# Optimization experiments

Measured on AMD Instinct MI355X. Metric: run time of the kernel, lower is better.

Reference implementation:

```python
import jax, jax.numpy as jnp
import numpy as np
import math

MU = 5; ETA = 1.0; ITERS = 3
SIGMA_C = 1.0; SIGMA_S = 1.6 * SIGMA_C
SIGMA_M = 3.0; RHO = 0.99; TAU = 0.7
MAX_T = int(math.floor(3 * SIGMA_C))  # 3
MAX_S = int(math.floor(3 * SIGMA_M))  # 9
DELTA = 1.0
B, C, X, Y = 4, 1, 512, 512


def _gpdf(v, sig):
    return math.exp(-v * v / (2.0 * sig * sig)) / (math.sqrt(2.0 * math.pi) * sig)


def _sobel(img):
    k = jnp.array([[-1., -2., -1.], [0., 0., 0.], [1., 2., 1.]], dtype=img.dtype)
    kern = jnp.stack([k, k.T])[:, None]  # [2,1,3,3] OIHW
    return jax.lax.conv_general_dilated(img, kern, (1, 1), [(1, 1), (1, 1)],
                                        dimension_numbers=('NCHW', 'OIHW', 'NCHW'))


def _gather_flat(arr, idx):
    # arr [b,c,x,y], idx int [b,x,y] flattened spatial index (px*Y+py)
    b, c, x, y = arr.shape
    flat = arr.reshape(b, c, x * y)
    idxb = jnp.broadcast_to(idx.reshape(b, 1, x * y), (b, c, x * y))
    return jnp.take_along_axis(flat, idxb, axis=2).reshape(b, c, x, y)


def _safe_norm(v):
    m = jnp.linalg.norm(v, axis=1, keepdims=True)
    return v / jnp.where(m == 0, 1.0, m)


def _etf(images):
    b, c, x, y = images.shape
    sob = _sobel(images)                                   # [b,2,x,y]
    mag = jnp.linalg.norm(sob, axis=1, keepdims=True)      # [b,1,x,y]
    mag = mag / jnp.max(mag)
    mag_p = jnp.pad(mag, ((0, 0), (0, 0), (MU, MU), (MU, MU)))
    sobel_X = mag[:, None]                                 # [b,1,1,x,y]
    tang = _safe_norm(jnp.stack([-sob[:, 1], sob[:, 0]], axis=1))
    K = 2 * MU + 1
    for _ in range(ITERS):
        for ori in ('V', 'H'):
            tang_p = jnp.pad(tang, ((0, 0), (0, 0), (MU, MU), (MU, MU)))
            tang_X = tang[:, None]                         # [b,1,2,x,y]
            if ori == 'V':
                tang_Y = jnp.stack([tang_p[:, :, i:i + x, MU:MU + y] for i in range(K)], axis=1)
                sobel_Y = jnp.stack([mag_p[:, :, i:i + x, MU:MU + y] for i in range(K)], axis=1)
            else:
                tang_Y = jnp.stack([tang_p[:, :, MU:MU + x, i:i + y] for i in range(K)], axis=1)
                sobel_Y = jnp.stack([mag_p[:, :, MU:MU + x, i:i + y] for i in range(K)], axis=1)
            # weight: magnitude term * direction term / 2
            w = (jnp.tanh(ETA * (sobel_Y - sobel_X)) + 1.0) \
                * jnp.sum(tang_X * tang_Y, axis=2, keepdims=True) * 0.5
            tang = _safe_norm(jnp.sum(tang_Y * w, axis=1))
    return tang


def _dog(images, etf):
    b, c, x, y = images.shape
    xi, yi = jnp.meshgrid(jnp.arange(x, dtype=images.dtype),
                          jnp.arange(y, dtype=images.dtype), indexing='ij')
    idx0 = jnp.broadcast_to(jnp.stack([xi, yi])[None], (b, 2, x, y))
    per = jnp.stack([-etf[:, 1], etf[:, 0]], axis=1)       # perpendicular to flow
    dog = jnp.zeros_like(images)
    tw = 0.0
    for t in range(-MAX_T, MAX_T + 1):
        pts = idx0 + DELTA * per * t
        px = jnp.round(jnp.clip(pts[:, 0], 0, x - 1)).astype(jnp.int32)
        py = jnp.round(jnp.clip(pts[:, 1], 0, y - 1)).astype(jnp.int32)
        il = _gather_flat(images, px * y + py)
        gw = _gpdf(t, SIGMA_C) - RHO * _gpdf(t, SIGMA_S)
        tw += gw
        dog = dog + il * gw
    return dog / tw


def _fdog_float(images):
    b, c, x, y = images.shape
    etf = _etf(images)
    dog = _dog(images, etf)
    fdog = jnp.zeros_like(images)
    tw = 0.0
    xi, yi = jnp.meshgrid(jnp.arange(x, dtype=jnp.int32),
                          jnp.arange(y, dtype=jnp.int32), indexing='ij')
    for s_dir in (-1, 1):
        px = jnp.broadcast_to(xi[None], (b, x, y))
        py = jnp.broadcast_to(yi[None], (b, x, y))
        for s in range(0 if s_dir == 1 else 1, MAX_S + 1):
            if s != 0:
                p_etf = _gather_flat(etf, px * y + py)     # flow at current points
                fx = px.astype(images.dtype) + DELTA * p_etf[:, 0] * s_dir
                fy = py.astype(images.dtype) + DELTA * p_etf[:, 1] * s_dir
                px = jnp.round(jnp.clip(fx, 0, x - 1)).astype(jnp.int32)
                py = jnp.round(jnp.clip(fy, 0, y - 1)).astype(jnp.int32)
            f_s = _gather_flat(dog, px * y + py)
            gw = _gpdf(s, SIGMA_M)
            tw += gw
            fdog = fdog + f_s * gw
    return fdog / tw


def setup_inputs() -> dict:
    key = jax.random.key(0)
    images = jax.random.uniform(key, (B, C, X, Y), dtype=jnp.float32)
    return {"images": images}


def reference(images):
    fdog = _fdog_float(images)
    edges = ~((fdog < 0) & (1.0 + jnp.tanh(fdog) < TAU))
    return edges.astype(jnp.int32)
```

## Files before the change

kernel.cpp:

```cpp
#include <hip/hip_runtime.h>
#include <math.h>

#pragma clang fp contract(off)

#define BN 4
#define SX 512
#define SY 512
#define NPIX (BN * SX * SY)
#define MU 5
#define MB (1024 * 1024)
#define NBLOCKS 4096

struct DogW  { float g[7];  float tw; };
struct FdogW { float g[10]; float tw; };

__device__ __forceinline__ float fast_tanh_f32(float dF) {
    double d = (double)dF;
    double y = fabs(d);
    double t = expm1(2.0 * y);
    double r = t / (t + 2.0);
    if (y > 350.0) r = 1.0;
    return (float)copysign(r, d);
}

__device__ __forceinline__ float img_at(const float* __restrict__ img, int b, int x, int y) {
    if (x < 0 || x >= SX || y < 0 || y >= SY) return 0.0f;
    return img[(size_t)b * SX * SY + (size_t)x * SY + y];
}

__global__ void k_sobel(const float* __restrict__ img, float* __restrict__ mag,
                        float2* __restrict__ tang, float* __restrict__ partial) {
#pragma clang fp contract(off)
    int yi = blockIdx.x * blockDim.x + threadIdx.x;
    int xi = blockIdx.y;
    int b  = blockIdx.z;

    float v00 = img_at(img, b, xi - 1, yi - 1);
    float v01 = img_at(img, b, xi - 1, yi    );
    float v02 = img_at(img, b, xi - 1, yi + 1);
    float v10 = img_at(img, b, xi,     yi - 1);
    float v12 = img_at(img, b, xi,     yi + 1);
    float v20 = img_at(img, b, xi + 1, yi - 1);
    float v21 = img_at(img, b, xi + 1, yi    );
    float v22 = img_at(img, b, xi + 1, yi + 1);

    float s0 = (-1.0f * v00);
    s0 = s0 + (-2.0f * v01);
    s0 = s0 + (-1.0f * v02);
    s0 = s0 + ( 1.0f * v20);
    s0 = s0 + ( 2.0f * v21);
    s0 = s0 + ( 1.0f * v22);
    float s1 = (-1.0f * v00);
    s1 = s1 + ( 1.0f * v02);
    s1 = s1 + (-2.0f * v10);
    s1 = s1 + ( 2.0f * v12);
    s1 = s1 + (-1.0f * v20);
    s1 = s1 + ( 1.0f * v22);

    float m = sqrtf((s0 * s0) + (s1 * s1));
    size_t idx = (size_t)b * SX * SY + (size_t)xi * SY + yi;
    mag[idx] = m;

    float tx = -s1, ty = s0;
    float n = sqrtf((tx * tx) + (ty * ty));
    float d = (n == 0.0f) ? 1.0f : n;
    tang[idx] = make_float2(tx / d, ty / d);

    float wm = m;
    for (int off = 32; off > 0; off >>= 1) wm = fmaxf(wm, __shfl_down(wm, off, 64));
    __shared__ float red[4];
    int lane = threadIdx.x & 63;
    int wid  = threadIdx.x >> 6;
    if (lane == 0) red[wid] = wm;
    __syncthreads();
    if (threadIdx.x == 0) {
        float bm = fmaxf(fmaxf(red[0], red[1]), fmaxf(red[2], red[3]));
        int bid = blockIdx.x + gridDim.x * (blockIdx.y + gridDim.y * blockIdx.z);
        partial[bid] = bm;
    }
}

__global__ void k_reduce(const float* __restrict__ partial, unsigned int* __restrict__ maxbits) {
    float m = 0.0f;
    for (int i = threadIdx.x; i < NBLOCKS; i += 256) m = fmaxf(m, partial[i]);
    for (int off = 32; off > 0; off >>= 1) m = fmaxf(m, __shfl_down(m, off, 64));
    __shared__ float red[4];
    int lane = threadIdx.x & 63;
    int wid  = threadIdx.x >> 6;
    if (lane == 0) red[wid] = m;
    __syncthreads();
    if (threadIdx.x == 0) {
        float bm = fmaxf(fmaxf(red[0], red[1]), fmaxf(red[2], red[3]));
        *maxbits = __float_as_uint(bm);
    }
}

__global__ void k_norm(float* __restrict__ mag, const unsigned int* __restrict__ maxbits) {
    int i = blockIdx.x * blockDim.x + threadIdx.x;
    float mx = __uint_as_float(*maxbits);
    mag[i] = mag[i] / mx;
}

__global__ void k_tanh(const float* __restrict__ mag, const unsigned int* __restrict__ maxbits,
                       float* __restrict__ TV, float* __restrict__ TH) {
#pragma clang fp contract(off)
    int yi = blockIdx.x * blockDim.x + threadIdx.x;
    int xi = blockIdx.y;
    int b  = blockIdx.z;
    size_t base = (size_t)b * SX * SY;
    size_t idx  = base + (size_t)xi * SY + yi;
    float mx = __uint_as_float(*maxbits);
    float cm = mag[idx] / mx;
#pragma unroll
    for (int k = 1; k <= 5; ++k) {
        if (xi + k < SX) {
            float nm = mag[idx + (size_t)k * SY] / mx;
            TV[(size_t)(k - 1) * NPIX + idx] = fast_tanh_f32(nm - cm);
        }
    }
#pragma unroll
    for (int k = 1; k <= 5; ++k) {
        if (yi + k < SY) {
            float nm = mag[idx + k] / mx;
            TH[(size_t)(k - 1) * NPIX + idx] = fast_tanh_f32(nm - cm);
        }
    }
}

#define VTY 32
#define VTX 8
__global__ __launch_bounds__(256) void k_etf_v(const float2* __restrict__ tsrc,
                                               float2* __restrict__ tdst,
                                               const float* __restrict__ TV) {
#pragma clang fp contract(off)
    int ty = threadIdx.x & 31;
    int tx = threadIdx.x >> 5;
    int y0 = blockIdx.x * VTY;
    int x0 = blockIdx.y * VTX;
    int b  = blockIdx.z;
    size_t base = (size_t)b * SX * SY;

    __shared__ __align__(16) float2 sT[VTX + 2 * MU][VTY];
    __shared__ __align__(16) float  sTV[5][VTX + MU][VTY];

    int tid = threadIdx.x;
    for (int i = tid; i < (VTX + 2 * MU) * (VTY / 2) / 2; i += 256) {
        break;
    }
    for (int i = tid; i < (VTX + 2 * MU) * (VTY / 4) * 2; i += 256) {
        int r = i >> 4;
        int c = i & 15;
        int gx = x0 - MU + r;
        if (gx >= 0 && gx < SX)
            ((float4*)&sT[r][0])[c] = ((const float4*)(tsrc + base + (size_t)gx * SY + y0))[c];
    }
    for (int i = tid; i < 5 * (VTX + MU) * (VTY / 4); i += 256) {
        int j   = i / ((VTX + MU) * (VTY / 4));
        int rem = i - j * ((VTX + MU) * (VTY / 4));
        int r   = rem >> 3;
        int c   = rem & 7;
        int gx  = x0 - MU + r;
        if (gx >= 0 && gx < SX)
            ((float4*)&sTV[j][r][0])[c] =
                ((const float4*)(TV + (size_t)j * NPIX + base + (size_t)gx * SY + y0))[c];
    }
    __syncthreads();

    int xi = x0 + tx;
    int yi = y0 + ty;
    size_t idx = base + (size_t)xi * SY + yi;

    float2 ct = sT[tx + MU][ty];

    float sx = 0.0f, sy = 0.0f;
#pragma unroll
    for (int k = -MU; k <= MU; ++k) {
        int nx = xi + k;
        if (nx < 0 || nx >= SX) continue;
        float2 nt = sT[tx + MU + k][ty];
        float th;
        if (k > 0)      th =  sTV[k - 1][tx + MU][ty];
        else if (k < 0) th = -sTV[-k - 1][tx + MU + k][ty];
        else            th =  0.0f;
        float dot = (ct.x * nt.x) + (ct.y * nt.y);
        float w   = ((th + 1.0f) * dot) * 0.5f;
        sx = sx + (nt.x * w);
        sy = sy + (nt.y * w);
    }
    float n = sqrtf((sx * sx) + (sy * sy));
    float d = (n == 0.0f) ? 1.0f : n;
    tdst[idx] = make_float2(sx / d, sy / d);
}

__global__ __launch_bounds__(256) void k_etf_h(const float2* __restrict__ tsrc,
                                               float2* __restrict__ tdst,
                                               const float* __restrict__ TH) {
#pragma clang fp contract(off)
    int tid = threadIdx.x;
    int xi  = blockIdx.y;
    int b   = blockIdx.z;
    size_t rowbase = (size_t)b * SX * SY + (size_t)xi * SY;

    __shared__ __align__(16) float2 sT[SY];
    __shared__ __align__(16) float  sTH[5][SY];

    ((float4*)sT)[tid] = ((const float4*)(tsrc + rowbase))[tid];
    for (int i = tid; i < 5 * (SY / 4); i += 256) {
        int j = i >> 7;
        int c = i & 127;
        ((float4*)&sTH[0][0])[i] = ((const float4*)(TH + (size_t)j * NPIX + rowbase))[c];
    }
    __syncthreads();

#pragma unroll
    for (int half = 0; half < 2; ++half) {
        int yi = tid + half * 256;
        float2 ct = sT[yi];
        float sx = 0.0f, sy = 0.0f;
#pragma unroll
        for (int k = -MU; k <= MU; ++k) {
            int ny = yi + k;
            if (ny < 0 || ny >= SY) continue;
            float2 nt = sT[ny];
            float th;
            if (k > 0)      th =  sTH[k - 1][yi];
            else if (k < 0) th = -sTH[-k - 1][ny];
            else            th =  0.0f;
            float dot = (ct.x * nt.x) + (ct.y * nt.y);
            float w   = ((th + 1.0f) * dot) * 0.5f;
            sx = sx + (nt.x * w);
            sy = sy + (nt.y * w);
        }
        float n = sqrtf((sx * sx) + (sy * sy));
        float d = (n == 0.0f) ? 1.0f : n;
        tdst[rowbase + yi] = make_float2(sx / d, sy / d);
    }
}

__global__ void k_etf(const float2* __restrict__ tsrc, float2* __restrict__ tdst,
                      const float* __restrict__ mag, int vert) {
#pragma clang fp contract(off)
    int yi = blockIdx.x * blockDim.x + threadIdx.x;
    int xi = blockIdx.y;
    int b  = blockIdx.z;
    size_t base = (size_t)b * SX * SY;
    size_t idx  = base + (size_t)xi * SY + yi;

    float  cm = mag[idx];
    float2 ct = tsrc[idx];

    float sx = 0.0f, sy = 0.0f;
    for (int k = -MU; k <= MU; ++k) {
        int nx = xi + (vert ? k : 0);
        int ny = yi + (vert ? 0 : k);
        if (nx < 0 || nx >= SX || ny < 0 || ny >= SY) continue;
        size_t nidx = base + (size_t)nx * SY + ny;
        float  nm = mag[nidx];
        float2 nt = tsrc[nidx];
        float dot = (ct.x * nt.x) + (ct.y * nt.y);
        float th  = (float)tanh((double)(nm - cm));
        float w   = ((th + 1.0f) * dot) * 0.5f;
        sx = sx + (nt.x * w);
        sy = sy + (nt.y * w);
    }
    float n = sqrtf((sx * sx) + (sy * sy));
    float d = (n == 0.0f) ? 1.0f : n;
    tdst[idx] = make_float2(sx / d, sy / d);
}

__global__ void k_dog(const float* __restrict__ img, const float2* __restrict__ etf,
                      float* __restrict__ dog, DogW w) {
#pragma clang fp contract(off)
    int yi = blockIdx.x * blockDim.x + threadIdx.x;
    int xi = blockIdx.y;
    int b  = blockIdx.z;
    size_t base = (size_t)b * SX * SY;
    size_t idx  = base + (size_t)xi * SY + yi;

    float2 e = etf[idx];
    float perx = -e.y;
    float pery =  e.x;
    float xf = (float)xi, yf = (float)yi;

    float acc = 0.0f;
#pragma unroll
    for (int t = -3; t <= 3; ++t) {
        float tf  = (float)t;
        float ptx = xf + (perx * tf);
        float pty = yf + (pery * tf);
        int px = (int)rintf(fminf(fmaxf(ptx, 0.0f), (float)(SX - 1)));
        int py = (int)rintf(fminf(fmaxf(pty, 0.0f), (float)(SY - 1)));
        float il = img[base + (size_t)px * SY + py];
        acc = acc + (il * w.g[t + 3]);
    }
    dog[idx] = acc / w.tw;
}

__global__ void k_fdog(const float* __restrict__ dog, const float2* __restrict__ etf,
                       int* __restrict__ out, FdogW w) {
#pragma clang fp contract(off)
    int yi = blockIdx.x * blockDim.x + threadIdx.x;
    int xi = blockIdx.y;
    int b  = blockIdx.z;
    size_t base = (size_t)b * SX * SY;
    size_t idx  = base + (size_t)xi * SY + yi;

    float d1[9];
    float d2[10];
    float2 e0 = etf[idx];
    float2 e1 = e0, e2 = e0;
    int p1x = xi, p1y = yi;
    int p2x = xi, p2y = yi;
    d2[0] = dog[idx];

#pragma unroll
    for (int s = 1; s <= 9; ++s) {
        float fx1 = (float)p1x + (e1.x * -1.0f);
        float fy1 = (float)p1y + (e1.y * -1.0f);
        p1x = (int)rintf(fminf(fmaxf(fx1, 0.0f), (float)(SX - 1)));
        p1y = (int)rintf(fminf(fmaxf(fy1, 0.0f), (float)(SY - 1)));
        size_t i1 = base + (size_t)p1x * SY + p1y;
        float fx2 = (float)p2x + (e2.x * 1.0f);
        float fy2 = (float)p2y + (e2.y * 1.0f);
        p2x = (int)rintf(fminf(fmaxf(fx2, 0.0f), (float)(SX - 1)));
        p2y = (int)rintf(fminf(fmaxf(fy2, 0.0f), (float)(SY - 1)));
        size_t i2 = base + (size_t)p2x * SY + p2y;

        d1[s - 1] = dog[i1];
        d2[s]     = dog[i2];
        if (s < 9) {
            e1 = etf[i1];
            e2 = etf[i2];
        }
    }

    float acc = 0.0f;
#pragma unroll
    for (int s = 1; s <= 9; ++s) acc = acc + (d1[s - 1] * w.g[s]);
    acc = acc + (d2[0] * w.g[0]);
#pragma unroll
    for (int s = 1; s <= 9; ++s) acc = acc + (d2[s] * w.g[s]);

    float fv = acc / w.tw;
    float th = 1.0f + fast_tanh_f32(fv);
    out[idx] = ((fv < 0.0f) && (th < 0.7f)) ? 0 : 1;
}

static double gpdf(double v, double sig) {
    return exp(-(v * v) / (2.0 * sig * sig)) / (sqrt(2.0 * M_PI) * sig);
}

extern "C" void kernel_launch(void* const* d_in, const int* in_sizes, int n_in,
                              void* d_out, int out_size, void* d_ws, size_t ws_size,
                              hipStream_t stream) {
    const float* img = (const float*)d_in[0];
    int* out = (int*)d_out;
    char* ws = (char*)d_ws;

    const size_t need = (size_t)60 * MB + NBLOCKS * sizeof(float) + 4;
    bool fast = ws_size >= need;

    float*  mag = (float*)(ws);
    float2* tA  = (float2*)(ws + (size_t)4  * MB);
    float2* tB  = (float2*)(ws + (size_t)12 * MB);
    float*  dog = (float*)(ws + (size_t)12 * MB);
    float*  TV  = (float*)(ws + (size_t)20 * MB);
    float*  TH  = (float*)(ws + (size_t)40 * MB);
    size_t  tail = fast ? (size_t)60 * MB : (size_t)20 * MB;
    float*        partial = (float*)(ws + tail);
    unsigned int* maxbits = (unsigned int*)(ws + tail + NBLOCKS * sizeof(float));

    dim3 blk(256, 1, 1);
    dim3 grd(SY / 256, SX, BN);
    dim3 vgrd(SY / VTY, SX / VTX, BN);
    dim3 hgrd(1, SX, BN);

    k_sobel<<<grd, blk, 0, stream>>>(img, mag, tA, partial);
    k_reduce<<<1, 256, 0, stream>>>(partial, maxbits);

    float2* src = tA;
    float2* dst = tB;
    if (fast) {
        k_tanh<<<grd, blk, 0, stream>>>(mag, maxbits, TV, TH);
        for (int it = 0; it < 3; ++it) {
            k_etf_v<<<vgrd, blk, 0, stream>>>(src, dst, TV);
            { float2* t = src; src = dst; dst = t; }
            k_etf_h<<<hgrd, blk, 0, stream>>>(src, dst, TH);
            { float2* t = src; src = dst; dst = t; }
        }
    } else {
        k_norm<<<NPIX / 256, 256, 0, stream>>>(mag, maxbits);
        for (int it = 0; it < 3; ++it) {
            k_etf<<<grd, blk, 0, stream>>>(src, dst, mag, 1);
            { float2* t = src; src = dst; dst = t; }
            k_etf<<<grd, blk, 0, stream>>>(src, dst, mag, 0);
            { float2* t = src; src = dst; dst = t; }
        }
    }
    float* dogbuf = (src == tA) ? dog : (float*)tA;

    DogW dw;
    {
        double tw = 0.0;
        for (int t = -3; t <= 3; ++t) {
            double g = gpdf((double)t, 1.0) - 0.99 * gpdf((double)t, 1.6);
            dw.g[t + 3] = (float)g;
            tw += g;
        }
        dw.tw = (float)tw;
    }
    k_dog<<<grd, blk, 0, stream>>>(img, src, dogbuf, dw);

    FdogW fw;
    {
        for (int s = 0; s <= 9; ++s) fw.g[s] = (float)gpdf((double)s, 3.0);
        double tw = 0.0;
        for (int s = 1; s <= 9; ++s) tw += gpdf((double)s, 3.0);
        for (int s = 0; s <= 9; ++s) tw += gpdf((double)s, 3.0);
        fw.tw = (float)tw;
    }
    k_fdog<<<grd, blk, 0, stream>>>(dogbuf, src, out, fw);
}
```

Measured before the change: 195.6 us.

## Remap all kernels to one row per block with slab-ordered grid

Every per-pixel kernel now uses a common 8x256 grid where each block handles a full 512-wide row (two halves per thread), and the slab-major blockIdx.x ordering interleaves batches and image halves. The vertical ETF kernel drops its shared-memory tile and reads neighbours and tanh weights straight from global memory, relying on cache reuse between adjacent rows. The aim is to improve cache locality across concurrently scheduled blocks and to halve the block count. The cost is less per-block parallelism and possibly more global-memory traffic in the vertical pass.

```diff
diff --git a/kernel.cpp b/kernel.cpp
--- a/kernel.cpp
+++ b/kernel.cpp
@@ -9,7 +9,7 @@
 #define NPIX (BN * SX * SY)
 #define MU 5
 #define MB (1024 * 1024)
-#define NBLOCKS 4096
+#define NBLOCKS 2048
 
 struct DogW  { float g[7];  float tw; };
 struct FdogW { float g[10]; float tw; };
@@ -28,55 +28,65 @@
     return img[(size_t)b * SX * SY + (size_t)x * SY + y];
 }
 
-__global__ void k_sobel(const float* __restrict__ img, float* __restrict__ mag,
-                        float2* __restrict__ tang, float* __restrict__ partial) {
-#pragma clang fp contract(off)
-    int yi = blockIdx.x * blockDim.x + threadIdx.x;
-    int xi = blockIdx.y;
-    int b  = blockIdx.z;
-
-    float v00 = img_at(img, b, xi - 1, yi - 1);
-    float v01 = img_at(img, b, xi - 1, yi    );
-    float v02 = img_at(img, b, xi - 1, yi + 1);
-    float v10 = img_at(img, b, xi,     yi - 1);
-    float v12 = img_at(img, b, xi,     yi + 1);
-    float v20 = img_at(img, b, xi + 1, yi - 1);
-    float v21 = img_at(img, b, xi + 1, yi    );
-    float v22 = img_at(img, b, xi + 1, yi + 1);
-
-    float s0 = (-1.0f * v00);
-    s0 = s0 + (-2.0f * v01);
-    s0 = s0 + (-1.0f * v02);
-    s0 = s0 + ( 1.0f * v20);
-    s0 = s0 + ( 2.0f * v21);
-    s0 = s0 + ( 1.0f * v22);
-    float s1 = (-1.0f * v00);
-    s1 = s1 + ( 1.0f * v02);
-    s1 = s1 + (-2.0f * v10);
-    s1 = s1 + ( 2.0f * v12);
-    s1 = s1 + (-1.0f * v20);
-    s1 = s1 + ( 1.0f * v22);
-
-    float m = sqrtf((s0 * s0) + (s1 * s1));
-    size_t idx = (size_t)b * SX * SY + (size_t)xi * SY + yi;
-    mag[idx] = m;
-
-    float tx = -s1, ty = s0;
-    float n = sqrtf((tx * tx) + (ty * ty));
-    float d = (n == 0.0f) ? 1.0f : n;
-    tang[idx] = make_float2(tx / d, ty / d);
-
-    float wm = m;
-    for (int off = 32; off > 0; off >>= 1) wm = fmaxf(wm, __shfl_down(wm, off, 64));
+#define SLAB_DECODE                                   \
+    int slab = blockIdx.x;                            \
+    int b    = slab >> 1;                             \
+    int xi   = ((slab & 1) << 8) + blockIdx.y;        \
+    size_t base = (size_t)b * SX * SY;                \
+    size_t rowb = base + (size_t)xi * SY;
+
+__global__ __launch_bounds__(256) void k_sobel(const float* __restrict__ img,
+                                               float* __restrict__ mag,
+                                               float2* __restrict__ tang,
+                                               float* __restrict__ partial) {
+#pragma clang fp contract(off)
+    SLAB_DECODE
+    float bmax = 0.0f;
+#pragma unroll
+    for (int half = 0; half < 2; ++half) {
+        int yi = (int)threadIdx.x + half * 256;
+
+        float v00 = img_at(img, b, xi - 1, yi - 1);
+        float v01 = img_at(img, b, xi - 1, yi    );
+        float v02 = img_at(img, b, xi - 1, yi + 1);
+        float v10 = img_at(img, b, xi,     yi - 1);
+        float v12 = img_at(img, b, xi,     yi + 1);
+        float v20 = img_at(img, b, xi + 1, yi - 1);
+        float v21 = img_at(img, b, xi + 1, yi    );
+        float v22 = img_at(img, b, xi + 1, yi + 1);
+
+        float s0 = (-1.0f * v00);
+        s0 = s0 + (-2.0f * v01);
+        s0 = s0 + (-1.0f * v02);
+        s0 = s0 + ( 1.0f * v20);
+        s0 = s0 + ( 2.0f * v21);
+        s0 = s0 + ( 1.0f * v22);
+        float s1 = (-1.0f * v00);
+        s1 = s1 + ( 1.0f * v02);
+        s1 = s1 + (-2.0f * v10);
+        s1 = s1 + ( 2.0f * v12);
+        s1 = s1 + (-1.0f * v20);
+        s1 = s1 + ( 1.0f * v22);
+
+        float m = sqrtf((s0 * s0) + (s1 * s1));
+        mag[rowb + yi] = m;
+
+        float tx = -s1, ty = s0;
+        float n = sqrtf((tx * tx) + (ty * ty));
+        float d = (n == 0.0f) ? 1.0f : n;
+        tang[rowb + yi] = make_float2(tx / d, ty / d);
+        bmax = fmaxf(bmax, m);
+    }
+
+    for (int off = 32; off > 0; off >>= 1) bmax = fmaxf(bmax, __shfl_down(bmax, off, 64));
     __shared__ float red[4];
     int lane = threadIdx.x & 63;
     int wid  = threadIdx.x >> 6;
-    if (lane == 0) red[wid] = wm;
+    if (lane == 0) red[wid] = bmax;
     __syncthreads();
     if (threadIdx.x == 0) {
         float bm = fmaxf(fmaxf(red[0], red[1]), fmaxf(red[2], red[3]));
-        int bid = blockIdx.x + gridDim.x * (blockIdx.y + gridDim.y * blockIdx.z);
-        partial[bid] = bm;
+        partial[blockIdx.x + 8 * blockIdx.y] = bm;
     }
 }
 
@@ -101,114 +111,82 @@
     mag[i] = mag[i] / mx;
 }
 
-__global__ void k_tanh(const float* __restrict__ mag, const unsigned int* __restrict__ maxbits,
-                       float* __restrict__ TV, float* __restrict__ TH) {
-#pragma clang fp contract(off)
-    int yi = blockIdx.x * blockDim.x + threadIdx.x;
-    int xi = blockIdx.y;
-    int b  = blockIdx.z;
-    size_t base = (size_t)b * SX * SY;
-    size_t idx  = base + (size_t)xi * SY + yi;
+__global__ __launch_bounds__(256) void k_tanh(const float* __restrict__ mag,
+                                              const unsigned int* __restrict__ maxbits,
+                                              float* __restrict__ TV, float* __restrict__ TH) {
+#pragma clang fp contract(off)
+    SLAB_DECODE
     float mx = __uint_as_float(*maxbits);
-    float cm = mag[idx] / mx;
-#pragma unroll
-    for (int k = 1; k <= 5; ++k) {
-        if (xi + k < SX) {
-            float nm = mag[idx + (size_t)k * SY] / mx;
-            TV[(size_t)(k - 1) * NPIX + idx] = fast_tanh_f32(nm - cm);
-        }
-    }
-#pragma unroll
-    for (int k = 1; k <= 5; ++k) {
-        if (yi + k < SY) {
-            float nm = mag[idx + k] / mx;
-            TH[(size_t)(k - 1) * NPIX + idx] = fast_tanh_f32(nm - cm);
-        }
-    }
-}
-
-#define VTY 32
-#define VTX 8
+#pragma unroll
+    for (int half = 0; half < 2; ++half) {
+        int yi = (int)threadIdx.x + half * 256;
+        size_t idx = rowb + yi;
+        float cm = mag[idx] / mx;
+#pragma unroll
+        for (int k = 1; k <= 5; ++k) {
+            if (xi + k < SX) {
+                float nm = mag[idx + (size_t)k * SY] / mx;
+                TV[(size_t)(k - 1) * NPIX + idx] = fast_tanh_f32(nm - cm);
+            }
+        }
+#pragma unroll
+        for (int k = 1; k <= 5; ++k) {
+            if (yi + k < SY) {
+                float nm = mag[idx + k] / mx;
+                TH[(size_t)(k - 1) * NPIX + idx] = fast_tanh_f32(nm - cm);
+            }
+        }
+    }
+}
+
 __global__ __launch_bounds__(256) void k_etf_v(const float2* __restrict__ tsrc,
                                                float2* __restrict__ tdst,
                                                const float* __restrict__ TV) {
 #pragma clang fp contract(off)
-    int ty = threadIdx.x & 31;
-    int tx = threadIdx.x >> 5;
-    int y0 = blockIdx.x * VTY;
-    int x0 = blockIdx.y * VTX;
-    int b  = blockIdx.z;
-    size_t base = (size_t)b * SX * SY;
-
-    __shared__ __align__(16) float2 sT[VTX + 2 * MU][VTY];
-    __shared__ __align__(16) float  sTV[5][VTX + MU][VTY];
-
-    int tid = threadIdx.x;
-    for (int i = tid; i < (VTX + 2 * MU) * (VTY / 2) / 2; i += 256) {
-        break;
-    }
-    for (int i = tid; i < (VTX + 2 * MU) * (VTY / 4) * 2; i += 256) {
-        int r = i >> 4;
-        int c = i & 15;
-        int gx = x0 - MU + r;
-        if (gx >= 0 && gx < SX)
-            ((float4*)&sT[r][0])[c] = ((const float4*)(tsrc + base + (size_t)gx * SY + y0))[c];
-    }
-    for (int i = tid; i < 5 * (VTX + MU) * (VTY / 4); i += 256) {
-        int j   = i / ((VTX + MU) * (VTY / 4));
-        int rem = i - j * ((VTX + MU) * (VTY / 4));
-        int r   = rem >> 3;
-        int c   = rem & 7;
-        int gx  = x0 - MU + r;
-        if (gx >= 0 && gx < SX)
-            ((float4*)&sTV[j][r][0])[c] =
-                ((const float4*)(TV + (size_t)j * NPIX + base + (size_t)gx * SY + y0))[c];
-    }
-    __syncthreads();
-
-    int xi = x0 + tx;
-    int yi = y0 + ty;
-    size_t idx = base + (size_t)xi * SY + yi;
-
-    float2 ct = sT[tx + MU][ty];
-
-    float sx = 0.0f, sy = 0.0f;
-#pragma unroll
-    for (int k = -MU; k <= MU; ++k) {
-        int nx = xi + k;
-        if (nx < 0 || nx >= SX) continue;
-        float2 nt = sT[tx + MU + k][ty];
-        float th;
-        if (k > 0)      th =  sTV[k - 1][tx + MU][ty];
-        else if (k < 0) th = -sTV[-k - 1][tx + MU + k][ty];
-        else            th =  0.0f;
-        float dot = (ct.x * nt.x) + (ct.y * nt.y);
-        float w   = ((th + 1.0f) * dot) * 0.5f;
-        sx = sx + (nt.x * w);
-        sy = sy + (nt.y * w);
-    }
-    float n = sqrtf((sx * sx) + (sy * sy));
-    float d = (n == 0.0f) ? 1.0f : n;
-    tdst[idx] = make_float2(sx / d, sy / d);
+    SLAB_DECODE
+#pragma unroll
+    for (int half = 0; half < 2; ++half) {
+        int yi = (int)threadIdx.x + half * 256;
+        size_t idx = rowb + yi;
+        float2 ct = tsrc[idx];
+
+        float sx = 0.0f, sy = 0.0f;
+#pragma unroll
+        for (int k = -MU; k <= MU; ++k) {
+            int nx = xi + k;
+            if (nx < 0 || nx >= SX) continue;
+            size_t nidx = idx + (size_t)k * SY;
+            float2 nt = tsrc[nidx];
+            float th;
+            if (k > 0)      th =  TV[(size_t)(k - 1) * NPIX + idx];
+            else if (k < 0) th = -TV[(size_t)(-k - 1) * NPIX + nidx];
+            else            th =  0.0f;
+            float dot = (ct.x * nt.x) + (ct.y * nt.y);
+            float w   = ((th + 1.0f) * dot) * 0.5f;
+            sx = sx + (nt.x * w);
+            sy = sy + (nt.y * w);
+        }
+        float n = sqrtf((sx * sx) + (sy * sy));
+        float d = (n == 0.0f) ? 1.0f : n;
+        tdst[idx] = make_float2(sx / d, sy / d);
+    }
 }
 
 __global__ __launch_bounds__(256) void k_etf_h(const float2* __restrict__ tsrc,
                                                float2* __restrict__ tdst,
                                                const float* __restrict__ TH) {
 #pragma clang fp contract(off)
+    SLAB_DECODE
     int tid = threadIdx.x;
-    int xi  = blockIdx.y;
-    int b   = blockIdx.z;
-    size_t rowbase = (size_t)b * SX * SY + (size_t)xi * SY;
 
     __shared__ __align__(16) float2 sT[SY];
     __shared__ __align__(16) float  sTH[5][SY];
 
-    ((float4*)sT)[tid] = ((const float4*)(tsrc + rowbase))[tid];
+    ((float4*)sT)[tid] = ((const float4*)(tsrc + rowb))[tid];
     for (int i = tid; i < 5 * (SY / 4); i += 256) {
         int j = i >> 7;
         int c = i & 127;
-        ((float4*)&sTH[0][0])[i] = ((const float4*)(TH + (size_t)j * NPIX + rowbase))[c];
+        ((float4*)&sTH[0][0])[i] = ((const float4*)(TH + (size_t)j * NPIX + rowb))[c];
     }
     __syncthreads();
 
@@ -233,7 +211,7 @@
         }
         float n = sqrtf((sx * sx) + (sy * sy));
         float d = (n == 0.0f) ? 1.0f : n;
-        tdst[rowbase + yi] = make_float2(sx / d, sy / d);
+        tdst[rowb + yi] = make_float2(sx / d, sy / d);
     }
 }
 
@@ -268,82 +246,85 @@
     tdst[idx] = make_float2(sx / d, sy / d);
 }
 
-__global__ void k_dog(const float* __restrict__ img, const float2* __restrict__ etf,
-                      float* __restrict__ dog, DogW w) {
-#pragma clang fp contract(off)
-    int yi = blockIdx.x * blockDim.x + threadIdx.x;
-    int xi = blockIdx.y;
-    int b  = blockIdx.z;
-    size_t base = (size_t)b * SX * SY;
-    size_t idx  = base + (size_t)xi * SY + yi;
-
-    float2 e = etf[idx];
-    float perx = -e.y;
-    float pery =  e.x;
-    float xf = (float)xi, yf = (float)yi;
-
-    float acc = 0.0f;
-#pragma unroll
-    for (int t = -3; t <= 3; ++t) {
-        float tf  = (float)t;
-        float ptx = xf + (perx * tf);
-        float pty = yf + (pery * tf);
-        int px = (int)rintf(fminf(fmaxf(ptx, 0.0f), (float)(SX - 1)));
-        int py = (int)rintf(fminf(fmaxf(pty, 0.0f), (float)(SY - 1)));
-        float il = img[base + (size_t)px * SY + py];
-        acc = acc + (il * w.g[t + 3]);
-    }
-    dog[idx] = acc / w.tw;
-}
-
-__global__ void k_fdog(const float* __restrict__ dog, const float2* __restrict__ etf,
-                       int* __restrict__ out, FdogW w) {
-#pragma clang fp contract(off)
-    int yi = blockIdx.x * blockDim.x + threadIdx.x;
-    int xi = blockIdx.y;
-    int b  = blockIdx.z;
-    size_t base = (size_t)b * SX * SY;
-    size_t idx  = base + (size_t)xi * SY + yi;
-
-    float d1[9];
-    float d2[10];
-    float2 e0 = etf[idx];
-    float2 e1 = e0, e2 = e0;
-    int p1x = xi, p1y = yi;
-    int p2x = xi, p2y = yi;
-    d2[0] = dog[idx];
-
-#pragma unroll
-    for (int s = 1; s <= 9; ++s) {
-        float fx1 = (float)p1x + (e1.x * -1.0f);
-        float fy1 = (float)p1y + (e1.y * -1.0f);
-        p1x = (int)rintf(fminf(fmaxf(fx1, 0.0f), (float)(SX - 1)));
-        p1y = (int)rintf(fminf(fmaxf(fy1, 0.0f), (float)(SY - 1)));
-        size_t i1 = base + (size_t)p1x * SY + p1y;
-        float fx2 = (float)p2x + (e2.x * 1.0f);
-        float fy2 = (float)p2y + (e2.y * 1.0f);
-        p2x = (int)rintf(fminf(fmaxf(fx2, 0.0f), (float)(SX - 1)));
-        p2y = (int)rintf(fminf(fmaxf(fy2, 0.0f), (float)(SY - 1)));
-        size_t i2 = base + (size_t)p2x * SY + p2y;
-
-        d1[s - 1] = dog[i1];
-        d2[s]     = dog[i2];
-        if (s < 9) {
-            e1 = etf[i1];
-            e2 = etf[i2];
-        }
-    }
-
-    float acc = 0.0f;
-#pragma unroll
-    for (int s = 1; s <= 9; ++s) acc = acc + (d1[s - 1] * w.g[s]);
-    acc = acc + (d2[0] * w.g[0]);
-#pragma unroll
-    for (int s = 1; s <= 9; ++s) acc = acc + (d2[s] * w.g[s]);
-
-    float fv = acc / w.tw;
-    float th = 1.0f + fast_tanh_f32(fv);
-    out[idx] = ((fv < 0.0f) && (th < 0.7f)) ? 0 : 1;
+__global__ __launch_bounds__(256) void k_dog(const float* __restrict__ img,
+                                             const float2* __restrict__ etf,
+                                             float* __restrict__ dog, DogW w) {
+#pragma clang fp contract(off)
+    SLAB_DECODE
+#pragma unroll
+    for (int half = 0; half < 2; ++half) {
+        int yi = (int)threadIdx.x + half * 256;
+        size_t idx = rowb + yi;
+
+        float2 e = etf[idx];
+        float perx = -e.y;
+        float pery =  e.x;
+        float xf = (float)xi, yf = (float)yi;
+
+        float acc = 0.0f;
+#pragma unroll
+        for (int t = -3; t <= 3; ++t) {
+            float tf  = (float)t;
+            float ptx = xf + (perx * tf);
+            float pty = yf + (pery * tf);
+            int px = (int)rintf(fminf(fmaxf(ptx, 0.0f), (float)(SX - 1)));
+            int py = (int)rintf(fminf(fmaxf(pty, 0.0f), (float)(SY - 1)));
+            float il = img[base + (size_t)px * SY + py];
+            acc = acc + (il * w.g[t + 3]);
+        }
+        dog[idx] = acc / w.tw;
+    }
+}
+
+__global__ __launch_bounds__(256) void k_fdog(const float* __restrict__ dog,
+                                              const float2* __restrict__ etf,
+                                              int* __restrict__ out, FdogW w) {
+#pragma clang fp contract(off)
+    SLAB_DECODE
+    for (int half = 0; half < 2; ++half) {
+        int yi = (int)threadIdx.x + half * 256;
+        size_t idx = rowb + yi;
+
+        float d1[9];
+        float d2[10];
+        float2 e0 = etf[idx];
+        float2 e1 = e0, e2 = e0;
+        int p1x = xi, p1y = yi;
+        int p2x = xi, p2y = yi;
+        d2[0] = dog[idx];
+
+#pragma unroll
+        for (int s = 1; s <= 9; ++s) {
+            float fx1 = (float)p1x + (e1.x * -1.0f);
+            float fy1 = (float)p1y + (e1.y * -1.0f);
+            p1x = (int)rintf(fminf(fmaxf(fx1, 0.0f), (float)(SX - 1)));
+            p1y = (int)rintf(fminf(fmaxf(fy1, 0.0f), (float)(SY - 1)));
+            size_t i1 = base + (size_t)p1x * SY + p1y;
+            float fx2 = (float)p2x + (e2.x * 1.0f);
+            float fy2 = (float)p2y + (e2.y * 1.0f);
+            p2x = (int)rintf(fminf(fmaxf(fx2, 0.0f), (float)(SX - 1)));
+            p2y = (int)rintf(fminf(fmaxf(fy2, 0.0f), (float)(SY - 1)));
+            size_t i2 = base + (size_t)p2x * SY + p2y;
+
+            d1[s - 1] = dog[i1];
+            d2[s]     = dog[i2];
+            if (s < 9) {
+                e1 = etf[i1];
+                e2 = etf[i2];
+            }
+        }
+
+        float acc = 0.0f;
+#pragma unroll
+        for (int s = 1; s <= 9; ++s) acc = acc + (d1[s - 1] * w.g[s]);
+        acc = acc + (d2[0] * w.g[0]);
+#pragma unroll
+        for (int s = 1; s <= 9; ++s) acc = acc + (d2[s] * w.g[s]);
+
+        float fv = acc / w.tw;
+        float th = 1.0f + fast_tanh_f32(fv);
+        out[idx] = ((fv < 0.0f) && (th < 0.7f)) ? 0 : 1;
+    }
 }
 
 static double gpdf(double v, double sig) {
@@ -371,24 +352,23 @@
     unsigned int* maxbits = (unsigned int*)(ws + tail + NBLOCKS * sizeof(float));
 
     dim3 blk(256, 1, 1);
-    dim3 grd(SY / 256, SX, BN);
-    dim3 vgrd(SY / VTY, SX / VTX, BN);
-    dim3 hgrd(1, SX, BN);
-
-    k_sobel<<<grd, blk, 0, stream>>>(img, mag, tA, partial);
+    dim3 sgrd(8, 256, 1);
+
+    k_sobel<<<sgrd, blk, 0, stream>>>(img, mag, tA, partial);
     k_reduce<<<1, 256, 0, stream>>>(partial, maxbits);
 
     float2* src = tA;
     float2* dst = tB;
     if (fast) {
-        k_tanh<<<grd, blk, 0, stream>>>(mag, maxbits, TV, TH);
+        k_tanh<<<sgrd, blk, 0, stream>>>(mag, maxbits, TV, TH);
         for (int it = 0; it < 3; ++it) {
-            k_etf_v<<<vgrd, blk, 0, stream>>>(src, dst, TV);
+            k_etf_v<<<sgrd, blk, 0, stream>>>(src, dst, TV);
             { float2* t = src; src = dst; dst = t; }
-            k_etf_h<<<hgrd, blk, 0, stream>>>(src, dst, TH);
+            k_etf_h<<<sgrd, blk, 0, stream>>>(src, dst, TH);
             { float2* t = src; src = dst; dst = t; }
         }
     } else {
+        dim3 grd(SY / 256, SX, BN);
         k_norm<<<NPIX / 256, 256, 0, stream>>>(mag, maxbits);
         for (int it = 0; it < 3; ++it) {
             k_etf<<<grd, blk, 0, stream>>>(src, dst, mag, 1);
@@ -409,7 +389,7 @@
         }
         dw.tw = (float)tw;
     }
-    k_dog<<<grd, blk, 0, stream>>>(img, src, dogbuf, dw);
+    k_dog<<<sgrd, blk, 0, stream>>>(img, src, dogbuf, dw);
 
     FdogW fw;
     {
@@ -419,5 +399,5 @@
         for (int s = 0; s <= 9; ++s) tw += gpdf((double)s, 3.0);
         fw.tw = (float)tw;
     }
-    k_fdog<<<grd, blk, 0, stream>>>(dogbuf, src, out, fw);
-}
+    k_fdog<<<sgrd, blk, 0, stream>>>(dogbuf, src, out, fw);
+}
```

Measured after the change: 205.5 us. +5.1%, slower.

## Replace shared-memory ETF tiles with direct per-thread global loads and clamped indices

Applied to the files above, without the earlier changes.

The vertical and horizontal ETF kernels drop their LDS tiling and syncthreads and instead issue all eleven neighbour loads per thread straight from global memory, using clamped indices and select-based masking in place of branches. Sobel and the tanh precompute are rewritten the same way, with loads hoisted ahead of the compute. The fallback path and the workspace-size check are removed, and dog gets its own buffer. This trades LDS staging and barrier cost for more global and cache traffic, and it assumes a workspace of at least 64 MB.

```diff
diff --git a/kernel.cpp b/kernel.cpp
--- a/kernel.cpp
+++ b/kernel.cpp
@@ -23,26 +23,40 @@
     return (float)copysign(r, d);
 }
 
-__device__ __forceinline__ float img_at(const float* __restrict__ img, int b, int x, int y) {
-    if (x < 0 || x >= SX || y < 0 || y >= SY) return 0.0f;
-    return img[(size_t)b * SX * SY + (size_t)x * SY + y];
-}
-
-__global__ void k_sobel(const float* __restrict__ img, float* __restrict__ mag,
-                        float2* __restrict__ tang, float* __restrict__ partial) {
-#pragma clang fp contract(off)
-    int yi = blockIdx.x * blockDim.x + threadIdx.x;
-    int xi = blockIdx.y;
-    int b  = blockIdx.z;
-
-    float v00 = img_at(img, b, xi - 1, yi - 1);
-    float v01 = img_at(img, b, xi - 1, yi    );
-    float v02 = img_at(img, b, xi - 1, yi + 1);
-    float v10 = img_at(img, b, xi,     yi - 1);
-    float v12 = img_at(img, b, xi,     yi + 1);
-    float v20 = img_at(img, b, xi + 1, yi - 1);
-    float v21 = img_at(img, b, xi + 1, yi    );
-    float v22 = img_at(img, b, xi + 1, yi + 1);
+__device__ __forceinline__ int clampi(int v, int lo, int hi) {
+    return v < lo ? lo : (v > hi ? hi : v);
+}
+
+__global__ __launch_bounds__(256) void k_sobel(const float* __restrict__ img,
+                                               float* __restrict__ mag,
+                                               float2* __restrict__ tang,
+                                               float* __restrict__ partial) {
+#pragma clang fp contract(off)
+    int yi = blockIdx.x * blockDim.x + threadIdx.x;
+    int xi = blockIdx.y;
+    int b  = blockIdx.z;
+    size_t base = (size_t)b * SX * SY;
+
+    int xm = clampi(xi - 1, 0, SX - 1), xp = clampi(xi + 1, 0, SX - 1);
+    int ym = clampi(yi - 1, 0, SY - 1), yp = clampi(yi + 1, 0, SY - 1);
+    float l00 = img[base + (size_t)xm * SY + ym];
+    float l01 = img[base + (size_t)xm * SY + yi];
+    float l02 = img[base + (size_t)xm * SY + yp];
+    float l10 = img[base + (size_t)xi * SY + ym];
+    float l12 = img[base + (size_t)xi * SY + yp];
+    float l20 = img[base + (size_t)xp * SY + ym];
+    float l21 = img[base + (size_t)xp * SY + yi];
+    float l22 = img[base + (size_t)xp * SY + yp];
+    bool vxm = (xi - 1) >= 0, vxp = (xi + 1) < SX;
+    bool vym = (yi - 1) >= 0, vyp = (yi + 1) < SY;
+    float v00 = (vxm && vym) ? l00 : 0.0f;
+    float v01 = (vxm       ) ? l01 : 0.0f;
+    float v02 = (vxm && vyp) ? l02 : 0.0f;
+    float v10 = (       vym) ? l10 : 0.0f;
+    float v12 = (       vyp) ? l12 : 0.0f;
+    float v20 = (vxp && vym) ? l20 : 0.0f;
+    float v21 = (vxp       ) ? l21 : 0.0f;
+    float v22 = (vxp && vyp) ? l22 : 0.0f;
 
     float s0 = (-1.0f * v00);
     s0 = s0 + (-2.0f * v01);
@@ -58,7 +72,7 @@
     s1 = s1 + ( 1.0f * v22);
 
     float m = sqrtf((s0 * s0) + (s1 * s1));
-    size_t idx = (size_t)b * SX * SY + (size_t)xi * SY + yi;
+    size_t idx = base + (size_t)xi * SY + yi;
     mag[idx] = m;
 
     float tx = -s1, ty = s0;
@@ -89,20 +103,13 @@
     int wid  = threadIdx.x >> 6;
     if (lane == 0) red[wid] = m;
     __syncthreads();
-    if (threadIdx.x == 0) {
-        float bm = fmaxf(fmaxf(red[0], red[1]), fmaxf(red[2], red[3]));
-        *maxbits = __float_as_uint(bm);
-    }
-}
-
-__global__ void k_norm(float* __restrict__ mag, const unsigned int* __restrict__ maxbits) {
-    int i = blockIdx.x * blockDim.x + threadIdx.x;
-    float mx = __uint_as_float(*maxbits);
-    mag[i] = mag[i] / mx;
-}
-
-__global__ void k_tanh(const float* __restrict__ mag, const unsigned int* __restrict__ maxbits,
-                       float* __restrict__ TV, float* __restrict__ TH) {
+    if (threadIdx.x == 0)
+        *maxbits = __float_as_uint(fmaxf(fmaxf(red[0], red[1]), fmaxf(red[2], red[3])));
+}
+
+__global__ __launch_bounds__(256) void k_tanh(const float* __restrict__ mag,
+                                              const unsigned int* __restrict__ maxbits,
+                                              float* __restrict__ TV, float* __restrict__ TH) {
 #pragma clang fp contract(off)
     int yi = blockIdx.x * blockDim.x + threadIdx.x;
     int xi = blockIdx.y;
@@ -110,82 +117,65 @@
     size_t base = (size_t)b * SX * SY;
     size_t idx  = base + (size_t)xi * SY + yi;
     float mx = __uint_as_float(*maxbits);
+
+    float mv[5], mh[5];
+#pragma unroll
+    for (int k = 1; k <= 5; ++k)
+        mv[k - 1] = mag[base + (size_t)clampi(xi + k, 0, SX - 1) * SY + yi];
+#pragma unroll
+    for (int k = 1; k <= 5; ++k)
+        mh[k - 1] = mag[base + (size_t)xi * SY + clampi(yi + k, 0, SY - 1)];
     float cm = mag[idx] / mx;
+
 #pragma unroll
     for (int k = 1; k <= 5; ++k) {
-        if (xi + k < SX) {
-            float nm = mag[idx + (size_t)k * SY] / mx;
-            TV[(size_t)(k - 1) * NPIX + idx] = fast_tanh_f32(nm - cm);
-        }
+        if (xi + k < SX)
+            TV[(size_t)(k - 1) * NPIX + idx] = fast_tanh_f32((mv[k - 1] / mx) - cm);
     }
 #pragma unroll
     for (int k = 1; k <= 5; ++k) {
-        if (yi + k < SY) {
-            float nm = mag[idx + k] / mx;
-            TH[(size_t)(k - 1) * NPIX + idx] = fast_tanh_f32(nm - cm);
-        }
-    }
-}
-
-#define VTY 32
-#define VTX 8
+        if (yi + k < SY)
+            TH[(size_t)(k - 1) * NPIX + idx] = fast_tanh_f32((mh[k - 1] / mx) - cm);
+    }
+}
+
 __global__ __launch_bounds__(256) void k_etf_v(const float2* __restrict__ tsrc,
                                                float2* __restrict__ tdst,
                                                const float* __restrict__ TV) {
 #pragma clang fp contract(off)
-    int ty = threadIdx.x & 31;
-    int tx = threadIdx.x >> 5;
-    int y0 = blockIdx.x * VTY;
-    int x0 = blockIdx.y * VTX;
-    int b  = blockIdx.z;
-    size_t base = (size_t)b * SX * SY;
-
-    __shared__ __align__(16) float2 sT[VTX + 2 * MU][VTY];
-    __shared__ __align__(16) float  sTV[5][VTX + MU][VTY];
-
-    int tid = threadIdx.x;
-    for (int i = tid; i < (VTX + 2 * MU) * (VTY / 2) / 2; i += 256) {
-        break;
-    }
-    for (int i = tid; i < (VTX + 2 * MU) * (VTY / 4) * 2; i += 256) {
-        int r = i >> 4;
-        int c = i & 15;
-        int gx = x0 - MU + r;
-        if (gx >= 0 && gx < SX)
-            ((float4*)&sT[r][0])[c] = ((const float4*)(tsrc + base + (size_t)gx * SY + y0))[c];
-    }
-    for (int i = tid; i < 5 * (VTX + MU) * (VTY / 4); i += 256) {
-        int j   = i / ((VTX + MU) * (VTY / 4));
-        int rem = i - j * ((VTX + MU) * (VTY / 4));
-        int r   = rem >> 3;
-        int c   = rem & 7;
-        int gx  = x0 - MU + r;
-        if (gx >= 0 && gx < SX)
-            ((float4*)&sTV[j][r][0])[c] =
-                ((const float4*)(TV + (size_t)j * NPIX + base + (size_t)gx * SY + y0))[c];
-    }
-    __syncthreads();
-
-    int xi = x0 + tx;
-    int yi = y0 + ty;
-    size_t idx = base + (size_t)xi * SY + yi;
-
-    float2 ct = sT[tx + MU][ty];
+    int yi = blockIdx.x * blockDim.x + threadIdx.x;
+    int xi = blockIdx.y;
+    int b  = blockIdx.z;
+    size_t base = (size_t)b * SX * SY;
+    size_t idx  = base + (size_t)xi * SY + yi;
+
+    float2 nt[11];
+    float  tv[11];
+#pragma unroll
+    for (int k = -MU; k <= MU; ++k) {
+        int nxc = clampi(xi + k, 0, SX - 1);
+        nt[k + MU] = tsrc[base + (size_t)nxc * SY + yi];
+        if (k > 0)      tv[k + MU] = TV[(size_t)(k - 1) * NPIX + idx];
+        else if (k < 0) tv[k + MU] = TV[(size_t)(-k - 1) * NPIX + base + (size_t)nxc * SY + yi];
+        else            tv[k + MU] = 0.0f;
+    }
+    float2 ct = nt[MU];
 
     float sx = 0.0f, sy = 0.0f;
 #pragma unroll
     for (int k = -MU; k <= MU; ++k) {
-        int nx = xi + k;
-        if (nx < 0 || nx >= SX) continue;
-        float2 nt = sT[tx + MU + k][ty];
+        bool valid = ((unsigned)(xi + k)) < (unsigned)SX;
+        float2 v = nt[k + MU];
+        float vx = valid ? v.x : 0.0f;
+        float vy = valid ? v.y : 0.0f;
         float th;
-        if (k > 0)      th =  sTV[k - 1][tx + MU][ty];
-        else if (k < 0) th = -sTV[-k - 1][tx + MU + k][ty];
-        else            th =  0.0f;
-        float dot = (ct.x * nt.x) + (ct.y * nt.y);
+        if (k > 0)      th = valid ?  tv[k + MU] : 0.0f;
+        else if (k < 0) th = valid ? -tv[k + MU] : 0.0f;
+        else            th = 0.0f;
+        float dot = (ct.x * vx) + (ct.y * vy);
         float w   = ((th + 1.0f) * dot) * 0.5f;
-        sx = sx + (nt.x * w);
-        sy = sy + (nt.y * w);
+        sx = sx + (vx * w);
+        sy = sy + (vy * w);
     }
     float n = sqrtf((sx * sx) + (sy * sy));
     float d = (n == 0.0f) ? 1.0f : n;
@@ -196,80 +186,49 @@
                                                float2* __restrict__ tdst,
                                                const float* __restrict__ TH) {
 #pragma clang fp contract(off)
-    int tid = threadIdx.x;
-    int xi  = blockIdx.y;
-    int b   = blockIdx.z;
-    size_t rowbase = (size_t)b * SX * SY + (size_t)xi * SY;
-
-    __shared__ __align__(16) float2 sT[SY];
-    __shared__ __align__(16) float  sTH[5][SY];
-
-    ((float4*)sT)[tid] = ((const float4*)(tsrc + rowbase))[tid];
-    for (int i = tid; i < 5 * (SY / 4); i += 256) {
-        int j = i >> 7;
-        int c = i & 127;
-        ((float4*)&sTH[0][0])[i] = ((const float4*)(TH + (size_t)j * NPIX + rowbase))[c];
-    }
-    __syncthreads();
-
-#pragma unroll
-    for (int half = 0; half < 2; ++half) {
-        int yi = tid + half * 256;
-        float2 ct = sT[yi];
-        float sx = 0.0f, sy = 0.0f;
-#pragma unroll
-        for (int k = -MU; k <= MU; ++k) {
-            int ny = yi + k;
-            if (ny < 0 || ny >= SY) continue;
-            float2 nt = sT[ny];
-            float th;
-            if (k > 0)      th =  sTH[k - 1][yi];
-            else if (k < 0) th = -sTH[-k - 1][ny];
-            else            th =  0.0f;
-            float dot = (ct.x * nt.x) + (ct.y * nt.y);
-            float w   = ((th + 1.0f) * dot) * 0.5f;
-            sx = sx + (nt.x * w);
-            sy = sy + (nt.y * w);
-        }
-        float n = sqrtf((sx * sx) + (sy * sy));
-        float d = (n == 0.0f) ? 1.0f : n;
-        tdst[rowbase + yi] = make_float2(sx / d, sy / d);
-    }
-}
-
-__global__ void k_etf(const float2* __restrict__ tsrc, float2* __restrict__ tdst,
-                      const float* __restrict__ mag, int vert) {
-#pragma clang fp contract(off)
-    int yi = blockIdx.x * blockDim.x + threadIdx.x;
-    int xi = blockIdx.y;
-    int b  = blockIdx.z;
-    size_t base = (size_t)b * SX * SY;
-    size_t idx  = base + (size_t)xi * SY + yi;
-
-    float  cm = mag[idx];
-    float2 ct = tsrc[idx];
+    int yi = blockIdx.x * blockDim.x + threadIdx.x;
+    int xi = blockIdx.y;
+    int b  = blockIdx.z;
+    size_t base = (size_t)b * SX * SY;
+    size_t rowb = base + (size_t)xi * SY;
+    size_t idx  = rowb + yi;
+
+    float2 nt[11];
+    float  tv[11];
+#pragma unroll
+    for (int k = -MU; k <= MU; ++k) {
+        int nyc = clampi(yi + k, 0, SY - 1);
+        nt[k + MU] = tsrc[rowb + nyc];
+        if (k > 0)      tv[k + MU] = TH[(size_t)(k - 1) * NPIX + idx];
+        else if (k < 0) tv[k + MU] = TH[(size_t)(-k - 1) * NPIX + rowb + nyc];
+        else            tv[k + MU] = 0.0f;
+    }
+    float2 ct = nt[MU];
 
     float sx = 0.0f, sy = 0.0f;
+#pragma unroll
     for (int k = -MU; k <= MU; ++k) {
-        int nx = xi + (vert ? k : 0);
-        int ny = yi + (vert ? 0 : k);
-        if (nx < 0 || nx >= SX || ny < 0 || ny >= SY) continue;
-        size_t nidx = base + (size_t)nx * SY + ny;
-        float  nm = mag[nidx];
-        float2 nt = tsrc[nidx];
-        float dot = (ct.x * nt.x) + (ct.y * nt.y);
-        float th  = (float)tanh((double)(nm - cm));
+        bool valid = ((unsigned)(yi + k)) < (unsigned)SY;
+        float2 v = nt[k + MU];
+        float vx = valid ? v.x : 0.0f;
+        float vy = valid ? v.y : 0.0f;
+        float th;
+        if (k > 0)      th = valid ?  tv[k + MU] : 0.0f;
+        else if (k < 0) th = valid ? -tv[k + MU] : 0.0f;
+        else            th = 0.0f;
+        float dot = (ct.x * vx) + (ct.y * vy);
         float w   = ((th + 1.0f) * dot) * 0.5f;
-        sx = sx + (nt.x * w);
-        sy = sy + (nt.y * w);
+        sx = sx + (vx * w);
+        sy = sy + (vy * w);
     }
     float n = sqrtf((sx * sx) + (sy * sy));
     float d = (n == 0.0f) ? 1.0f : n;
     tdst[idx] = make_float2(sx / d, sy / d);
 }
 
-__global__ void k_dog(const float* __restrict__ img, const float2* __restrict__ etf,
-                      float* __restrict__ dog, DogW w) {
+__global__ __launch_bounds__(256) void k_dog(const float* __restrict__ img,
+                                             const float2* __restrict__ etf,
+                                             float* __restrict__ dog, DogW w) {
 #pragma clang fp contract(off)
     int yi = blockIdx.x * blockDim.x + threadIdx.x;
     int xi = blockIdx.y;
@@ -282,7 +241,7 @@
     float pery =  e.x;
     float xf = (float)xi, yf = (float)yi;
 
-    float acc = 0.0f;
+    float il[7];
 #pragma unroll
     for (int t = -3; t <= 3; ++t) {
         float tf  = (float)t;
@@ -290,14 +249,17 @@
         float pty = yf + (pery * tf);
         int px = (int)rintf(fminf(fmaxf(ptx, 0.0f), (float)(SX - 1)));
         int py = (int)rintf(fminf(fmaxf(pty, 0.0f), (float)(SY - 1)));
-        float il = img[base + (size_t)px * SY + py];
-        acc = acc + (il * w.g[t + 3]);
-    }
+        il[t + 3] = img[base + (size_t)px * SY + py];
+    }
+    float acc = 0.0f;
+#pragma unroll
+    for (int t = -3; t <= 3; ++t) acc = acc + (il[t + 3] * w.g[t + 3]);
     dog[idx] = acc / w.tw;
 }
 
-__global__ void k_fdog(const float* __restrict__ dog, const float2* __restrict__ etf,
-                       int* __restrict__ out, FdogW w) {
+__global__ __launch_bounds__(256) void k_fdog(const float* __restrict__ dog,
+                                              const float2* __restrict__ etf,
+                                              int* __restrict__ out, FdogW w) {
 #pragma clang fp contract(off)
     int yi = blockIdx.x * blockDim.x + threadIdx.x;
     int xi = blockIdx.y;
@@ -357,47 +319,14 @@
     int* out = (int*)d_out;
     char* ws = (char*)d_ws;
 
-    const size_t need = (size_t)60 * MB + NBLOCKS * sizeof(float) + 4;
-    bool fast = ws_size >= need;
-
     float*  mag = (float*)(ws);
     float2* tA  = (float2*)(ws + (size_t)4  * MB);
     float2* tB  = (float2*)(ws + (size_t)12 * MB);
-    float*  dog = (float*)(ws + (size_t)12 * MB);
     float*  TV  = (float*)(ws + (size_t)20 * MB);
     float*  TH  = (float*)(ws + (size_t)40 * MB);
-    size_t  tail = fast ? (size_t)60 * MB : (size_t)20 * MB;
-    float*        partial = (float*)(ws + tail);
-    unsigned int* maxbits = (unsigned int*)(ws + tail + NBLOCKS * sizeof(float));
-
-    dim3 blk(256, 1, 1);
-    dim3 grd(SY / 256, SX, BN);
-    dim3 vgrd(SY / VTY, SX / VTX, BN);
-    dim3 hgrd(1, SX, BN);
-
-    k_sobel<<<grd, blk, 0, stream>>>(img, mag, tA, partial);
-    k_reduce<<<1, 256, 0, stream>>>(partial, maxbits);
-
-    float2* src = tA;
-    float2* dst = tB;
-    if (fast) {
-        k_tanh<<<grd, blk, 0, stream>>>(mag, maxbits, TV, TH);
-        for (int it = 0; it < 3; ++it) {
-            k_etf_v<<<vgrd, blk, 0, stream>>>(src, dst, TV);
-            { float2* t = src; src = dst; dst = t; }
-            k_etf_h<<<hgrd, blk, 0, stream>>>(src, dst, TH);
-            { float2* t = src; src = dst; dst = t; }
-        }
-    } else {
-        k_norm<<<NPIX / 256, 256, 0, stream>>>(mag, maxbits);
-        for (int it = 0; it < 3; ++it) {
-            k_etf<<<grd, blk, 0, stream>>>(src, dst, mag, 1);
-            { float2* t = src; src = dst; dst = t; }
-            k_etf<<<grd, blk, 0, stream>>>(src, dst, mag, 0);
-            { float2* t = src; src = dst; dst = t; }
-        }
-    }
-    float* dogbuf = (src == tA) ? dog : (float*)tA;
+    float*  dog = (float*)(ws + (size_t)60 * MB);
+    float*        partial = (float*)(ws + (size_t)64 * MB);
+    unsigned int* maxbits = (unsigned int*)(ws + (size_t)64 * MB + NBLOCKS * sizeof(float));
 
     DogW dw;
     {
@@ -409,8 +338,6 @@
         }
         dw.tw = (float)tw;
     }
-    k_dog<<<grd, blk, 0, stream>>>(img, src, dogbuf, dw);
-
     FdogW fw;
     {
         for (int s = 0; s <= 9; ++s) fw.g[s] = (float)gpdf((double)s, 3.0);
@@ -419,5 +346,22 @@
         for (int s = 0; s <= 9; ++s) tw += gpdf((double)s, 3.0);
         fw.tw = (float)tw;
     }
-    k_fdog<<<grd, blk, 0, stream>>>(dogbuf, src, out, fw);
-}
+
+    dim3 blk(256, 1, 1);
+    dim3 grd(SY / 256, SX, BN);
+
+    k_sobel<<<grd, blk, 0, stream>>>(img, mag, tA, partial);
+    k_reduce<<<1, 256, 0, stream>>>(partial, maxbits);
+    k_tanh<<<grd, blk, 0, stream>>>(mag, maxbits, TV, TH);
+
+    float2* src = tA;
+    float2* dst = tB;
+    for (int it = 0; it < 3; ++it) {
+        k_etf_v<<<grd, blk, 0, stream>>>(src, dst, TV);
+        { float2* t = src; src = dst; dst = t; }
+        k_etf_h<<<grd, blk, 0, stream>>>(src, dst, TH);
+        { float2* t = src; src = dst; dst = t; }
+    }
+    k_dog<<<grd, blk, 0, stream>>>(img, src, dog, dw);
+    k_fdog<<<grd, blk, 0, stream>>>(dog, src, out, fw);
+}
```

Measured after the change: 201.5 us. 1.03x slower.
